# Kernel optimization log

Measured on AMD Instinct MI355X. Metric: run time of the kernel, lower is better.

## Reference

```python
import jax, jax.numpy as jnp
import numpy as np

EPS = 1e-5
SLOPE = 0.2
K = 20
B, N = 8, 2048

def _lrelu(x):
    return jnp.where(x >= 0, x, SLOPE * x)

def _bn(x, g, b, m, v, axis):
    # eval-mode batchnorm with running stats
    shape = [1] * x.ndim
    shape[axis] = -1
    g, b, m, v = (t.reshape(shape) for t in (g, b, m, v))
    return g * (x - m) * jax.lax.rsqrt(v + EPS) + b

def _knn(x, k):
    # x: (B, C, N) -> neighbor indices (B, N, k) by largest negative sq dist
    xx = jnp.sum(x * x, axis=1)                      # (B, N)
    inner = jnp.einsum('bcn,bcm->bnm', x, x)         # (B, N, N)
    pd = 2.0 * inner - xx[:, :, None] - xx[:, None, :]
    return jax.lax.top_k(pd, k)[1]

def _graph_feature(x, k):
    # x: (B, C, N) -> (B, 2C, N, k) edge features [nbr - center, center]
    idx = _knn(x, k)                                  # (B, N, k)
    xt = jnp.transpose(x, (0, 2, 1))                  # (B, N, C)
    nbr = xt[jnp.arange(x.shape[0])[:, None, None], idx]  # (B, N, k, C)
    center = xt[:, :, None, :]
    f = jnp.concatenate([nbr - center, jnp.broadcast_to(center, nbr.shape)], axis=-1)
    return jnp.transpose(f, (0, 3, 1, 2))

def _edge_block(x, W, g, b, m, v):
    f = _graph_feature(x, K)                          # (B, 2C, N, k)
    h = jnp.einsum('oc,bcnk->bonk', W, f)             # 1x1 conv
    return jnp.max(_lrelu(_bn(h, g, b, m, v, 1)), axis=-1)

def _forward(x, W1, bn1_g, bn1_b, bn1_m, bn1_v, W2, bn2_g, bn2_b, bn2_m, bn2_v, W3, bn3_g, bn3_b, bn3_m, bn3_v, W4, bn4_g, bn4_b, bn4_m, bn4_v, l1_w, l1_b, bn5_g, bn5_b, bn5_m, bn5_v, l2_w, l2_b, bn6_g, bn6_b, bn6_m, bn6_v, l3_w, l3_b):
    xc = jnp.transpose(x, (0, 2, 1))                  # (B, 3, N)
    x1 = _edge_block(xc, W1, bn1_g, bn1_b, bn1_m, bn1_v)   # (B, 64, N)
    x2 = _edge_block(x1, W2, bn2_g, bn2_b, bn2_m, bn2_v)   # (B, 64, N)
    x3 = _edge_block(x2, W3, bn3_g, bn3_b, bn3_m, bn3_v)   # (B, 128, N)
    h = jnp.concatenate([x1, x2, x3], axis=1)         # (B, 256, N)
    h = _lrelu(_bn(jnp.einsum('oc,bcn->bon', W4, h), bn4_g, bn4_b, bn4_m, bn4_v, 1))
    h = jnp.max(h, axis=-1)                           # (B, 1024)
    h = _lrelu(_bn(h @ l1_w.T + l1_b, bn5_g, bn5_b, bn5_m, bn5_v, 1))
    h = _lrelu(_bn(h @ l2_w.T + l2_b, bn6_g, bn6_b, bn6_m, bn6_v, 1))
    return h @ l3_w.T + l3_b                          # (B, 2)

def setup_inputs() -> dict:
    key = jax.random.key(0)
    ks = iter(jax.random.split(key, 64))
    def rn(shape, s=1.0):
        return jax.random.normal(next(ks), shape, jnp.float32) * s
    def add_bn(inp, prefix, c):
        inp[prefix + '_g'] = jax.random.uniform(next(ks), (c,), jnp.float32, 0.5, 1.5)
        inp[prefix + '_b'] = rn((c,), 0.1)
        inp[prefix + '_m'] = rn((c,), 0.1)
        inp[prefix + '_v'] = jax.random.uniform(next(ks), (c,), jnp.float32, 0.5, 1.5)
    inp = {'x': rn((B, N, 3))}
    inp['W1'] = rn((64, 6), 0.3); add_bn(inp, 'bn1', 64)
    inp['W2'] = rn((64, 128), 0.1); add_bn(inp, 'bn2', 64)
    inp['W3'] = rn((128, 128), 0.1); add_bn(inp, 'bn3', 128)
    inp['W4'] = rn((1024, 256), 0.08); add_bn(inp, 'bn4', 1024)
    inp['l1_w'] = rn((512, 1024), 0.03); inp['l1_b'] = rn((512,), 0.01); add_bn(inp, 'bn5', 512)
    inp['l2_w'] = rn((256, 512), 0.05); inp['l2_b'] = rn((256,), 0.01); add_bn(inp, 'bn6', 256)
    inp['l3_w'] = rn((2, 256), 0.06); inp['l3_b'] = rn((2,), 0.01)
    return inp

def reference(x, W1, bn1_g, bn1_b, bn1_m, bn1_v, W2, bn2_g, bn2_b, bn2_m, bn2_v, W3, bn3_g, bn3_b, bn3_m, bn3_v, W4, bn4_g, bn4_b, bn4_m, bn4_v, l1_w, l1_b, bn5_g, bn5_b, bn5_m, bn5_v, l2_w, l2_b, bn6_g, bn6_b, bn6_m, bn6_v, l3_w, l3_b):
    return _forward(x, W1, bn1_g, bn1_b, bn1_m, bn1_v, W2, bn2_g, bn2_b, bn2_m, bn2_v, W3, bn3_g, bn3_b, bn3_m, bn3_v, W4, bn4_g, bn4_b, bn4_m, bn4_v, l1_w, l1_b, bn5_g, bn5_b, bn5_m, bn5_v, l2_w, l2_b, bn6_g, bn6_b, bn6_m, bn6_v, l3_w, l3_b)
```

## Files before the change

### kernel.cpp

```cpp
#include <hip/hip_runtime.h>
#include <math.h>

#define NN 2048
#define KK 20
#define EPSF 1e-5f

__device__ __forceinline__ float lrelu(float v){ return v >= 0.f ? v : 0.2f*v; }

__device__ __forceinline__ void topk20_insert(float d, int idc, float (&v)[KK], int (&id)[KK]){
#pragma unroll
  for (int j = KK-1; j >= 1; --j){
    bool cjm1 = d > v[j-1];
    bool cj   = d > v[j];
    float nv = cjm1 ? v[j-1] : (cj ? d   : v[j]);
    int   ni = cjm1 ? id[j-1] : (cj ? idc : id[j]);
    v[j] = nv; id[j] = ni;
  }
  if (d > v[0]) { v[0] = d; id[0] = idc; }
}

__global__ void k_prep1(const float* __restrict__ x, const float* __restrict__ W1,
                        float* __restrict__ Y, float* __restrict__ T, float* __restrict__ SQ){
  __shared__ float wa[64][3], wd[64][3];
  int t = threadIdx.x;
  if (t < 64){
#pragma unroll
    for (int c=0;c<3;c++){
      float a = W1[t*6+c], b2 = W1[t*6+3+c];
      wa[t][c] = a; wd[t][c] = b2 - a;
    }
  }
  __syncthreads();
  int gid = blockIdx.x*256 + t;
  int b = gid >> 11, n = gid & (NN-1);
  float px = x[gid*3+0], py = x[gid*3+1], pz = x[gid*3+2];
  SQ[gid] = px*px + py*py + pz*pz;
  float* yb = Y + ((size_t)b*128)*NN + n;
  float* tb = T + ((size_t)b*128)*NN + n;
#pragma unroll 8
  for (int o=0;o<64;o++){
    yb[(size_t)o*NN] = wa[o][0]*px + wa[o][1]*py + wa[o][2]*pz;
    tb[(size_t)o*NN] = wd[o][0]*px + wd[o][1]*py + wd[o][2]*pz;
  }
}

__global__ __launch_bounds__(256) void k_knn3_part(const float* __restrict__ x, const float* __restrict__ SQ,
                                                   float* __restrict__ PV, unsigned short* __restrict__ PI){
  __shared__ __align__(16) float cd[128*4];
  int t = threadIdx.x;
  int half = blockIdx.x & 1, nb = blockIdx.x >> 1;
  int b = blockIdx.y;
  int n_base = nb * 32;
  int cbase = half * 1024;
  int ql = t & 31, sp = t >> 5;
  int n = n_base + ql;
  int gq = b*NN + n;
  float qx = x[gq*3], qy = x[gq*3+1], qz = x[gq*3+2];
  float qs = SQ[gq];
  float v[KK]; int id[KK];
#pragma unroll
  for (int i=0;i<KK;i++){ v[i] = -INFINITY; id[i] = 0; }
  int mlo = sp * 16;
  for (int tile=0; tile<8; ++tile){
    int m0 = cbase + tile * 128;
    __syncthreads();
#pragma unroll
    for (int i=0;i<2;i++){
      int f2 = t + i*256;
      int m = f2 >> 2, ch = f2 & 3;
      int gm = b*NN + m0 + m;
      cd[f2] = (ch < 3) ? x[gm*3 + ch] : SQ[gm];
    }
    __syncthreads();
    for (int j=mlo; j<mlo+16; ++j){
      float4 c4 = *(const float4*)&cd[j*4];
      float d = 2.f*(qx*c4.x + qy*c4.y + qz*c4.z) - qs - c4.w;
      if (d > v[KK-1]) topk20_insert(d, m0 + j, v, id);
    }
  }
  size_t base = ((size_t)b*16 + half*8 + sp)*KK;
#pragma unroll
  for (int r=0;r<KK;r++){
    PV[(base + r)*NN + n] = v[r];
    PI[(base + r)*NN + n] = (unsigned short)id[r];
  }
}

__global__ void k_sqnorm(const float* __restrict__ X, float* __restrict__ SQ){
  int gid = blockIdx.x*256 + threadIdx.x;
  int b = gid >> 11, n = gid & (NN-1);
  const float* xb = X + (size_t)b*256*NN;
  float s = 0.f;
#pragma unroll
  for (int c=0;c<64;c++){ float vv = xb[(size_t)c*NN + n]; s += vv*vv; }
  SQ[gid] = s;
}

__global__ __launch_bounds__(256) void k_knn64_part(const float* __restrict__ X, const float* __restrict__ SQ,
                                                    float* __restrict__ PV, unsigned short* __restrict__ PI){
  __shared__ __align__(16) float cd[64*68];
  __shared__ float cs_[64];
  int t = threadIdx.x;
  int half = blockIdx.x & 1, nb = blockIdx.x >> 1;
  int b = blockIdx.y;
  int n_base = nb * 32;
  int cbase = half * 1024;
  int ql = t & 31, sp = t >> 5;
  int n = n_base + ql;
  const float* xb = X + (size_t)b*256*NN;
  float q[64];
#pragma unroll
  for (int c=0;c<64;c++) q[c] = xb[(size_t)c*NN + n];
  float qs = SQ[b*NN + n];
  float v[KK]; int id[KK];
#pragma unroll
  for (int i=0;i<KK;i++){ v[i]=-INFINITY; id[i]=0; }
  int jlo = sp * 8;
  for (int tile=0; tile<16; ++tile){
    int m0 = cbase + tile*64;
    __syncthreads();
#pragma unroll
    for (int i=0;i<16;i++){
      int flat = i*256 + t;
      int c = flat >> 6, m = flat & 63;
      cd[m*68 + c] = xb[(size_t)c*NN + m0 + m];
    }
    if (t < 64) cs_[t] = SQ[b*NN + m0 + t];
    __syncthreads();
    for (int j=jlo; j<jlo+8; ++j){
      const float* crow = cd + j*68;
      float d = 0.f;
#pragma unroll
      for (int c=0;c<64;c+=4){
        float4 c4 = *(const float4*)&crow[c];
        d += q[c]*c4.x + q[c+1]*c4.y + q[c+2]*c4.z + q[c+3]*c4.w;
      }
      d = 2.f*d - qs - cs_[j];
      if (d > v[KK-1]) topk20_insert(d, m0 + j, v, id);
    }
  }
  size_t base = ((size_t)b*16 + half*8 + sp)*KK;
#pragma unroll
  for (int r=0;r<KK;r++){
    PV[(base + r)*NN + n] = v[r];
    PI[(base + r)*NN + n] = (unsigned short)id[r];
  }
}

__global__ void k_topk_merge16(const float* __restrict__ PV, const unsigned short* __restrict__ PI,
                               int* __restrict__ IDX){
  int gid = blockIdx.x*256 + threadIdx.x;
  int b = gid >> 11, n = gid & (NN-1);
  float hv[16]; int hi_[16]; int hp[16];
#pragma unroll
  for (int s=0;s<16;s++){
    hp[s] = 0;
    hv[s] = PV[(((size_t)b*16 + s)*KK)*NN + n];
    hi_[s] = (int)PI[(((size_t)b*16 + s)*KK)*NN + n];
  }
  for (int r=0;r<KK;r++){
    float bv = hv[0]; int bi = hi_[0]; int bs = 0;
#pragma unroll
    for (int s=1;s<16;s++){
      bool win = (hv[s] > bv) || ((hv[s] == bv) && (hi_[s] < bi));
      bv = win ? hv[s] : bv; bi = win ? hi_[s] : bi; bs = win ? s : bs;
    }
    IDX[((size_t)b*KK + r)*NN + n] = bi;
#pragma unroll
    for (int s=0;s<16;s++){
      if (s == bs){
        int np = hp[s] + 1; hp[s] = np;
        bool ok = np < KK;
        hv[s]  = ok ? PV[(((size_t)b*16 + s)*KK + np)*NN + n] : -INFINITY;
        hi_[s] = ok ? (int)PI[(((size_t)b*16 + s)*KK + np)*NN + n] : 0x7FFFFFFF;
      }
    }
  }
}

__global__ __launch_bounds__(256) void k_edge_apply(const float* __restrict__ Y, const float* __restrict__ T,
                             const int* __restrict__ IDX,
                             const float* __restrict__ g, const float* __restrict__ be,
                             const float* __restrict__ mu, const float* __restrict__ va,
                             float* __restrict__ OUT, int c_off){
  int t = threadIdx.x;
  int nl = t & 127, oh = t >> 7;
  int n = blockIdx.x*128 + nl;
  int b = blockIdx.z;
  int o0 = blockIdx.y*32 + oh*16;
  int idx[KK];
#pragma unroll
  for (int k2=0;k2<KK;k2++) idx[k2] = IDX[((size_t)b*KK + k2)*NN + n];
  for (int oo=0;oo<16;oo++){
    int o = o0 + oo;
    const float* yrow = Y + ((size_t)b*128 + o)*NN;
    float M = -INFINITY;
#pragma unroll
    for (int k2=0;k2<KK;k2++) M = fmaxf(M, yrow[idx[k2]]);
    float s = g[o] * rsqrtf(va[o] + EPSF);
    float val = s*(M + T[((size_t)b*128 + o)*NN + n] - mu[o]) + be[o];
    OUT[((size_t)b*256 + c_off + o)*NN + n] = lrelu(val);
  }
}

template<int O>
__global__ __launch_bounds__(256) void k_yt_gemm(const float* __restrict__ X, const float* __restrict__ W,
                                                 float* __restrict__ Y, float* __restrict__ T){
  __shared__ __align__(16) float wa[O][64];
  __shared__ __align__(16) float wd[O][64];
  int t = threadIdx.x;
  for (int i=t; i<O*64; i+=256){
    int o = i >> 6, c = i & 63;
    float a = W[o*128 + c];
    wa[o][c] = a;
    wd[o][c] = W[o*128 + 64 + c] - a;
  }
  __syncthreads();
  int half = t >> 7, ln = t & 127;
  int gid = blockIdx.x*128 + ln;
  int b = gid >> 11, n = gid & (NN-1);
  const float* xb = X + (size_t)b*256*NN;
  float q[64];
#pragma unroll
  for (int c=0;c<64;c++) q[c] = xb[(size_t)c*NN + n];
  int o0 = half * (O/2);
  for (int o=o0; o<o0+O/2; ++o){
    float ay=0.f, at=0.f;
#pragma unroll
    for (int c=0;c<64;c+=4){
      float4 a4 = *(const float4*)&wa[o][c];
      float4 d4 = *(const float4*)&wd[o][c];
      ay += a4.x*q[c] + a4.y*q[c+1] + a4.z*q[c+2] + a4.w*q[c+3];
      at += d4.x*q[c] + d4.y*q[c+1] + d4.z*q[c+2] + d4.w*q[c+3];
    }
    Y[((size_t)b*128 + o)*NN + n] = ay;
    T[((size_t)b*128 + o)*NN + n] = at;
  }
}

__global__ __launch_bounds__(256) void k_w4t(const float* __restrict__ W4, float* __restrict__ W4T){
  __shared__ float Tt[64][65];
  int t = threadIdx.x;
  int c0 = blockIdx.x * 64, o0 = blockIdx.y * 64;
#pragma unroll
  for (int p=0;p<16;p++){
    int f = p*256 + t;
    int i = f >> 6, j = f & 63;
    Tt[i][j] = W4[(size_t)(o0+i)*256 + c0 + j];
  }
  __syncthreads();
#pragma unroll
  for (int p=0;p<16;p++){
    int f = p*256 + t;
    int i = f >> 6, j = f & 63;
    W4T[(size_t)(c0+i)*1024 + o0 + j] = Tt[j][i];
  }
}

__global__ __launch_bounds__(256) void k_w4max(const float* __restrict__ CAT, const float* __restrict__ W4T,
                                               float* __restrict__ PART){
  __shared__ __align__(16) float wt[32][132];
  __shared__ __align__(16) float ct[32][132];
  int t = threadIdx.x;
  int io = t >> 4, in_ = t & 15;
  int nb = blockIdx.x * 128, ob = blockIdx.y * 128, b = blockIdx.z;
  const float* catb = CAT + (size_t)b*256*NN;
  float acc[8][8];
#pragma unroll
  for (int r=0;r<8;r++)
#pragma unroll
    for (int c=0;c<8;c++) acc[r][c]=0.f;
  for (int c0=0; c0<256; c0+=32){
    __syncthreads();
#pragma unroll
    for (int p=0;p<4;p++){
      int idx = p*256 + t;
      int cc = idx >> 5, o4 = (idx & 31) * 4;
      *(float4*)&wt[cc][o4] = *(const float4*)&W4T[(size_t)(c0+cc)*1024 + ob + o4];
    }
#pragma unroll
    for (int p=0;p<4;p++){
      int idx = p*256 + t;
      int cc = idx >> 5, n4 = (idx & 31) * 4;
      *(float4*)&ct[cc][n4] = *(const float4*)&catb[(size_t)(c0+cc)*NN + nb + n4];
    }
    __syncthreads();
#pragma unroll 4
    for (int c=0;c<32;c++){
      float4 a0 = *(const float4*)&wt[c][io*8];
      float4 a1 = *(const float4*)&wt[c][io*8+4];
      float4 b0 = *(const float4*)&ct[c][in_*8];
      float4 b1 = *(const float4*)&ct[c][in_*8+4];
      float ar[8] = {a0.x,a0.y,a0.z,a0.w,a1.x,a1.y,a1.z,a1.w};
      float br[8] = {b0.x,b0.y,b0.z,b0.w,b1.x,b1.y,b1.z,b1.w};
#pragma unroll
      for (int r=0;r<8;r++)
#pragma unroll
        for (int s=0;s<8;s++) acc[r][s] += ar[r]*br[s];
    }
  }
#pragma unroll
  for (int r=0;r<8;r++){
    float m = acc[r][0];
#pragma unroll
    for (int s=1;s<8;s++) m = fmaxf(m, acc[r][s]);
    m = fmaxf(m, __shfl_xor(m, 1));
    m = fmaxf(m, __shfl_xor(m, 2));
    m = fmaxf(m, __shfl_xor(m, 4));
    m = fmaxf(m, __shfl_xor(m, 8));
    if (in_ == 0){
      int o = ob + io*8 + r;
      PART[((size_t)b*1024 + o)*16 + blockIdx.x] = m;
    }
  }
}

__global__ void k_reduce4(const float* __restrict__ PART,
                          const float* __restrict__ g, const float* __restrict__ be,
                          const float* __restrict__ mu, const float* __restrict__ va,
                          float* __restrict__ H4){
  int gid = blockIdx.x*256 + threadIdx.x;
  int o = gid & 1023;
  float M = -INFINITY;
#pragma unroll
  for (int i=0;i<16;i++) M = fmaxf(M, PART[(size_t)gid*16 + i]);
  float s = g[o]*rsqrtf(va[o]+EPSF);
  H4[gid] = lrelu(s*(M - mu[o]) + be[o]);
}

__global__ __launch_bounds__(256) void k_mlp(const float* __restrict__ H4,
      const float* __restrict__ l1w, const float* __restrict__ l1b,
      const float* __restrict__ g5, const float* __restrict__ b5,
      const float* __restrict__ m5, const float* __restrict__ v5,
      const float* __restrict__ l2w, const float* __restrict__ l2b,
      const float* __restrict__ g6, const float* __restrict__ b6,
      const float* __restrict__ m6, const float* __restrict__ v6,
      const float* __restrict__ l3w, const float* __restrict__ l3b,
      float* __restrict__ out){
  __shared__ float h[1024];
  __shared__ float h5[512];
  __shared__ float h6[256];
  int b = blockIdx.x, t = threadIdx.x;
  for (int i=t;i<1024;i+=256) h[i] = H4[b*1024+i];
  __syncthreads();
  for (int o=t;o<512;o+=256){
    float acc = l1b[o];
    for (int c=0;c<1024;c+=4){
      float4 w = *(const float4*)&l1w[(size_t)o*1024 + c];
      acc += w.x*h[c] + w.y*h[c+1] + w.z*h[c+2] + w.w*h[c+3];
    }
    float s = g5[o]*rsqrtf(v5[o]+EPSF);
    h5[o] = lrelu(s*(acc - m5[o]) + b5[o]);
  }
  __syncthreads();
  if (t < 256){
    int o = t;
    float acc = l2b[o];
    for (int c=0;c<512;c+=4){
      float4 w = *(const float4*)&l2w[(size_t)o*512 + c];
      acc += w.x*h5[c] + w.y*h5[c+1] + w.z*h5[c+2] + w.w*h5[c+3];
    }
    float s = g6[o]*rsqrtf(v6[o]+EPSF);
    h6[o] = lrelu(s*(acc - m6[o]) + b6[o]);
  }
  __syncthreads();
  if (t < 128){
    int o = t >> 6, l = t & 63;
    float p = 0.f;
#pragma unroll
    for (int j=0;j<4;j++){ int c = j*64 + l; p += l3w[o*256 + c]*h6[c]; }
    p += __shfl_xor(p, 32); p += __shfl_xor(p, 16); p += __shfl_xor(p, 8);
    p += __shfl_xor(p, 4);  p += __shfl_xor(p, 2);  p += __shfl_xor(p, 1);
    if (l == 0) out[b*2 + o] = p + l3b[o];
  }
}

extern "C" void kernel_launch(void* const* d_in, const int* in_sizes, int n_in,
                              void* d_out, int out_size, void* d_ws, size_t ws_size,
                              hipStream_t stream){
  (void)in_sizes; (void)n_in; (void)out_size; (void)ws_size;
  const float* x    = (const float*)d_in[0];
  const float* W1   = (const float*)d_in[1];
  const float* bn1g = (const float*)d_in[2];
  const float* bn1b = (const float*)d_in[3];
  const float* bn1m = (const float*)d_in[4];
  const float* bn1v = (const float*)d_in[5];
  const float* W2   = (const float*)d_in[6];
  const float* bn2g = (const float*)d_in[7];
  const float* bn2b = (const float*)d_in[8];
  const float* bn2m = (const float*)d_in[9];
  const float* bn2v = (const float*)d_in[10];
  const float* W3   = (const float*)d_in[11];
  const float* bn3g = (const float*)d_in[12];
  const float* bn3b = (const float*)d_in[13];
  const float* bn3m = (const float*)d_in[14];
  const float* bn3v = (const float*)d_in[15];
  const float* W4   = (const float*)d_in[16];
  const float* bn4g = (const float*)d_in[17];
  const float* bn4b = (const float*)d_in[18];
  const float* bn4m = (const float*)d_in[19];
  const float* bn4v = (const float*)d_in[20];
  const float* l1w  = (const float*)d_in[21];
  const float* l1b  = (const float*)d_in[22];
  const float* bn5g = (const float*)d_in[23];
  const float* bn5b = (const float*)d_in[24];
  const float* bn5m = (const float*)d_in[25];
  const float* bn5v = (const float*)d_in[26];
  const float* l2w  = (const float*)d_in[27];
  const float* l2b  = (const float*)d_in[28];
  const float* bn6g = (const float*)d_in[29];
  const float* bn6b = (const float*)d_in[30];
  const float* bn6m = (const float*)d_in[31];
  const float* bn6v = (const float*)d_in[32];
  const float* l3w  = (const float*)d_in[33];
  const float* l3b  = (const float*)d_in[34];

  float* CAT  = (float*)d_ws;
  float* Yb   = CAT + (size_t)8*256*NN;
  float* Tb   = Yb  + (size_t)8*128*NN;
  float* SQ   = Tb  + (size_t)8*128*NN;
  int*   IDX  = (int*)(SQ + (size_t)8*NN);
  float* PART = (float*)(IDX + (size_t)8*KK*NN);
  float* H4   = PART + (size_t)8*1024*16;
  float* W4T  = H4 + (size_t)8*1024;
  float* PTV  = W4T + (size_t)256*1024;
  unsigned short* PTI = (unsigned short*)(PTV + (size_t)8*16*KK*NN);

  k_w4t<<<dim3(4,16),256,0,stream>>>(W4, W4T);
  k_prep1<<<64,256,0,stream>>>(x, W1, Yb, Tb, SQ);
  k_knn3_part<<<dim3(128,8),256,0,stream>>>(x, SQ, PTV, PTI);
  k_topk_merge16<<<64,256,0,stream>>>(PTV, PTI, IDX);
  k_edge_apply<<<dim3(16,2,8),256,0,stream>>>(Yb, Tb, IDX, bn1g, bn1b, bn1m, bn1v, CAT, 0);
  k_sqnorm<<<64,256,0,stream>>>(CAT, SQ);
  k_knn64_part<<<dim3(128,8),256,0,stream>>>(CAT, SQ, PTV, PTI);
  k_topk_merge16<<<64,256,0,stream>>>(PTV, PTI, IDX);
  k_yt_gemm<64><<<128,256,0,stream>>>(CAT, W2, Yb, Tb);
  k_edge_apply<<<dim3(16,2,8),256,0,stream>>>(Yb, Tb, IDX, bn2g, bn2b, bn2m, bn2v, CAT, 64);
  k_sqnorm<<<64,256,0,stream>>>(CAT + (size_t)64*NN, SQ);
  k_knn64_part<<<dim3(128,8),256,0,stream>>>(CAT + (size_t)64*NN, SQ, PTV, PTI);
  k_topk_merge16<<<64,256,0,stream>>>(PTV, PTI, IDX);
  k_yt_gemm<128><<<128,256,0,stream>>>(CAT + (size_t)64*NN, W3, Yb, Tb);
  k_edge_apply<<<dim3(16,4,8),256,0,stream>>>(Yb, Tb, IDX, bn3g, bn3b, bn3m, bn3v, CAT, 128);
  k_w4max<<<dim3(16,8,8),256,0,stream>>>(CAT, W4T, PART);
  k_reduce4<<<32,256,0,stream>>>(PART, bn4g, bn4b, bn4m, bn4v, H4);
  k_mlp<<<8,256,0,stream>>>(H4, l1w, l1b, bn5g, bn5b, bn5m, bn5v,
                            l2w, l2b, bn6g, bn6b, bn6m, bn6v, l3w, l3b, (float*)d_out);
}
```

Baseline: 1.466 ms.

## Split 64-dim kNN into register-tiled Gram GEMM plus streaming top-k selection

Measured after the change: 1.425 ms. -2.8%, faster.

```diff
diff --git a/kernel.cpp b/kernel.cpp
--- a/kernel.cpp
+++ b/kernel.cpp
@@ -96,50 +96,89 @@
   SQ[gid] = s;
 }
 
-__global__ __launch_bounds__(256) void k_knn64_part(const float* __restrict__ X, const float* __restrict__ SQ,
-                                                    float* __restrict__ PV, unsigned short* __restrict__ PI){
-  __shared__ __align__(16) float cd[64*68];
-  __shared__ float cs_[64];
-  int t = threadIdx.x;
-  int half = blockIdx.x & 1, nb = blockIdx.x >> 1;
+__global__ __launch_bounds__(256) void k_gram(const float* __restrict__ X, float* __restrict__ D, int mh){
+  __shared__ __align__(16) float am[32][132];
+  __shared__ __align__(16) float bn[32][132];
+  int t = threadIdx.x;
+  int io = t >> 4, in_ = t & 15;
+  int nb = blockIdx.x * 128;
+  int mb = blockIdx.y * 128;
+  int b = blockIdx.z;
+  const float* xb = X + (size_t)b*256*NN;
+  int mg = mh*1024 + mb;
+  float acc[8][8];
+#pragma unroll
+  for (int r=0;r<8;r++)
+#pragma unroll
+    for (int c=0;c<8;c++) acc[r][c]=0.f;
+  for (int c0=0; c0<64; c0+=32){
+    __syncthreads();
+#pragma unroll
+    for (int p=0;p<4;p++){
+      int idx = p*256 + t;
+      int cc = idx >> 5, m4 = (idx & 31) * 4;
+      *(float4*)&am[cc][m4] = *(const float4*)&xb[(size_t)(c0+cc)*NN + mg + m4];
+    }
+#pragma unroll
+    for (int p=0;p<4;p++){
+      int idx = p*256 + t;
+      int cc = idx >> 5, n4 = (idx & 31) * 4;
+      *(float4*)&bn[cc][n4] = *(const float4*)&xb[(size_t)(c0+cc)*NN + nb + n4];
+    }
+    __syncthreads();
+#pragma unroll 4
+    for (int c=0;c<32;c++){
+      float4 a0 = *(const float4*)&am[c][io*8];
+      float4 a1 = *(const float4*)&am[c][io*8+4];
+      float4 b0 = *(const float4*)&bn[c][in_*8];
+      float4 b1 = *(const float4*)&bn[c][in_*8+4];
+      float ar[8] = {a0.x,a0.y,a0.z,a0.w,a1.x,a1.y,a1.z,a1.w};
+      float br[8] = {b0.x,b0.y,b0.z,b0.w,b1.x,b1.y,b1.z,b1.w};
+#pragma unroll
+      for (int r=0;r<8;r++)
+#pragma unroll
+        for (int s=0;s<8;s++) acc[r][s] += ar[r]*br[s];
+    }
+  }
+#pragma unroll
+  for (int r=0;r<8;r++){
+    size_t row = ((size_t)b*1024 + mb + io*8 + r)*NN + nb + in_*8;
+    *(float4*)&D[row]   = make_float4(acc[r][0],acc[r][1],acc[r][2],acc[r][3]);
+    *(float4*)&D[row+4] = make_float4(acc[r][4],acc[r][5],acc[r][6],acc[r][7]);
+  }
+}
+
+__global__ __launch_bounds__(256) void k_sel1024(const float* __restrict__ D, const float* __restrict__ SQ,
+                                                 int mh, float* __restrict__ PV, unsigned short* __restrict__ PI){
+  int t = threadIdx.x;
+  int q = t & 31, sp = t >> 5;
   int b = blockIdx.y;
-  int n_base = nb * 32;
-  int cbase = half * 1024;
-  int ql = t & 31, sp = t >> 5;
-  int n = n_base + ql;
-  const float* xb = X + (size_t)b*256*NN;
-  float q[64];
-#pragma unroll
-  for (int c=0;c<64;c++) q[c] = xb[(size_t)c*NN + n];
+  int n = blockIdx.x*32 + q;
   float qs = SQ[b*NN + n];
+  const float* drow = D + ((size_t)b*1024 + sp*128)*NN + n;
+  const float* sqb  = SQ + b*NN + mh*1024 + sp*128;
+  int idb = mh*1024 + sp*128;
   float v[KK]; int id[KK];
 #pragma unroll
   for (int i=0;i<KK;i++){ v[i]=-INFINITY; id[i]=0; }
-  int jlo = sp * 8;
-  for (int tile=0; tile<16; ++tile){
-    int m0 = cbase + tile*64;
-    __syncthreads();
-#pragma unroll
-    for (int i=0;i<16;i++){
-      int flat = i*256 + t;
-      int c = flat >> 6, m = flat & 63;
-      cd[m*68 + c] = xb[(size_t)c*NN + m0 + m];
-    }
-    if (t < 64) cs_[t] = SQ[b*NN + m0 + t];
-    __syncthreads();
-    for (int j=jlo; j<jlo+8; ++j){
-      const float* crow = cd + j*68;
-      float d = 0.f;
-#pragma unroll
-      for (int c=0;c<64;c+=4){
-        float4 c4 = *(const float4*)&crow[c];
-        d += q[c]*c4.x + q[c+1]*c4.y + q[c+2]*c4.z + q[c+3]*c4.w;
-      }
-      d = 2.f*d - qs - cs_[j];
-      if (d > v[KK-1]) topk20_insert(d, m0 + j, v, id);
-    }
-  }
-  size_t base = ((size_t)b*16 + half*8 + sp)*KK;
+  float dk[8];
+#pragma unroll
+  for (int k=0;k<8;k++) dk[k] = drow[(size_t)k*NN];
+  for (int i=0;i<128;i+=8){
+    float nk[8];
+    if (i + 8 < 128){
+#pragma unroll
+      for (int k=0;k<8;k++) nk[k] = drow[(size_t)(i+8+k)*NN];
+    }
+#pragma unroll
+    for (int k=0;k<8;k++){
+      float d = 2.f*dk[k] - qs - sqb[i+k];
+      if (d > v[KK-1]) topk20_insert(d, idb + i + k, v, id);
+    }
+#pragma unroll
+    for (int k=0;k<8;k++) dk[k] = nk[k];
+  }
+  size_t base = ((size_t)b*16 + mh*8 + sp)*KK;
 #pragma unroll
   for (int r=0;r<KK;r++){
     PV[(base + r)*NN + n] = v[r];
@@ -425,6 +464,7 @@
   float* W4T  = H4 + (size_t)8*1024;
   float* PTV  = W4T + (size_t)256*1024;
   unsigned short* PTI = (unsigned short*)(PTV + (size_t)8*16*KK*NN);
+  float* D    = (float*)(PTI + (size_t)8*16*KK*NN);
 
   k_w4t<<<dim3(4,16),256,0,stream>>>(W4, W4T);
   k_prep1<<<64,256,0,stream>>>(x, W1, Yb, Tb, SQ);
@@ -432,12 +472,18 @@
   k_topk_merge16<<<64,256,0,stream>>>(PTV, PTI, IDX);
   k_edge_apply<<<dim3(16,2,8),256,0,stream>>>(Yb, Tb, IDX, bn1g, bn1b, bn1m, bn1v, CAT, 0);
   k_sqnorm<<<64,256,0,stream>>>(CAT, SQ);
-  k_knn64_part<<<dim3(128,8),256,0,stream>>>(CAT, SQ, PTV, PTI);
+  k_gram<<<dim3(16,8,8),256,0,stream>>>(CAT, D, 0);
+  k_sel1024<<<dim3(64,8),256,0,stream>>>(D, SQ, 0, PTV, PTI);
+  k_gram<<<dim3(16,8,8),256,0,stream>>>(CAT, D, 1);
+  k_sel1024<<<dim3(64,8),256,0,stream>>>(D, SQ, 1, PTV, PTI);
   k_topk_merge16<<<64,256,0,stream>>>(PTV, PTI, IDX);
   k_yt_gemm<64><<<128,256,0,stream>>>(CAT, W2, Yb, Tb);
   k_edge_apply<<<dim3(16,2,8),256,0,stream>>>(Yb, Tb, IDX, bn2g, bn2b, bn2m, bn2v, CAT, 64);
   k_sqnorm<<<64,256,0,stream>>>(CAT + (size_t)64*NN, SQ);
-  k_knn64_part<<<dim3(128,8),256,0,stream>>>(CAT + (size_t)64*NN, SQ, PTV, PTI);
+  k_gram<<<dim3(16,8,8),256,0,stream>>>(CAT + (size_t)64*NN, D, 0);
+  k_sel1024<<<dim3(64,8),256,0,stream>>>(D, SQ, 0, PTV, PTI);
+  k_gram<<<dim3(16,8,8),256,0,stream>>>(CAT + (size_t)64*NN, D, 1);
+  k_sel1024<<<dim3(64,8),256,0,stream>>>(D, SQ, 1, PTV, PTI);
   k_topk_merge16<<<64,256,0,stream>>>(PTV, PTI, IDX);
   k_yt_gemm<128><<<128,256,0,stream>>>(CAT + (size_t)64*NN, W3, Yb, Tb);
   k_edge_apply<<<dim3(16,4,8),256,0,stream>>>(Yb, Tb, IDX, bn3g, bn3b, bn3m, bn3v, CAT, 128);
```
